# Kernel optimization log

Measured on AMD Instinct MI355X. Metric: run time of the kernel, lower is better.

The kernel has to match this reference:

```python
import jax, jax.numpy as jnp
from jax import lax
import numpy as np

N = 10000      # num_nodes
T = 24         # hist_len
IN_DIM = 16
HID = 128
HEADS = 4
E = 160000     # num_edges
PRED = 24
NEG_SLOPE = 0.2  # GATv2 LeakyReLU default


def _lstm_layer(xs, wih, whh, bih, bhh):
    # xs: [T, N, D]; PyTorch gate order i, f, g, o
    Hh = whh.shape[1]
    h0 = jnp.zeros((xs.shape[1], Hh), xs.dtype)
    def step(carry, xt):
        h, c = carry
        g = xt @ wih.T + bih + h @ whh.T + bhh
        i, f, gg, o = jnp.split(g, 4, axis=-1)
        c = jax.nn.sigmoid(f) * c + jax.nn.sigmoid(i) * jnp.tanh(gg)
        h = jax.nn.sigmoid(o) * jnp.tanh(c)
        return (h, c), h
    (_, _), out = lax.scan(step, (h0, h0), xs)
    return out  # [T, N, Hh]


def _gatv2(z, src, dst, wl, bl, wr, br, att, bias):
    # PyG GATv2Conv: share_weights=False, concat=True, add_self_loops=False
    n = z.shape[0]
    xl = (z @ wl.T + bl).reshape(n, HEADS, HID)   # source/message transform
    xr = (z @ wr.T + br).reshape(n, HEADS, HID)   # target transform
    e = jax.nn.leaky_relu(xl[src] + xr[dst], NEG_SLOPE)   # [E, H, C]
    score = jnp.einsum('ehc,hc->eh', e, att)              # [E, H]
    smax = jax.ops.segment_max(score, dst, num_segments=n)
    p = jnp.exp(score - smax[dst])
    denom = jax.ops.segment_sum(p, dst, num_segments=n)
    alpha = p / (denom[dst] + 1e-16)                      # segment softmax over in-edges
    out = jax.ops.segment_sum(xl[src] * alpha[:, :, None], dst, num_segments=n)
    return out.reshape(n, HEADS * HID) + bias


def setup_inputs() -> dict:
    key = jax.random.key(0)
    ks = iter(jax.random.split(key, 64))
    def W(shape):
        return jax.random.normal(next(ks), shape, jnp.float32) / np.sqrt(shape[-1])
    inp = {}
    inp['x'] = jax.random.normal(next(ks), (N, T, IN_DIM), jnp.float32)
    inp['edge_index'] = jax.random.randint(next(ks), (2, E), 0, N, jnp.int32)
    inp['mlp_in_w0'] = W((HID, IN_DIM)); inp['mlp_in_b0'] = jnp.zeros((HID,), jnp.float32)
    inp['mlp_in_w1'] = W((HID, HID));    inp['mlp_in_b1'] = jnp.zeros((HID,), jnp.float32)
    for l in range(2):  # nn.LSTM(num_layers = lstm_num_layers*2 = 2)
        inp[f'lstm_wih{l}'] = W((4 * HID, HID))
        inp[f'lstm_whh{l}'] = W((4 * HID, HID))
        inp[f'lstm_bih{l}'] = jnp.zeros((4 * HID,), jnp.float32)
        inp[f'lstm_bhh{l}'] = jnp.zeros((4 * HID,), jnp.float32)
    for l in range(2):  # nGAT_layer = 2
        inp[f'gat{l}_wl'] = W((HEADS * HID, HID))
        inp[f'gat{l}_bl'] = jnp.zeros((HEADS * HID,), jnp.float32)
        inp[f'gat{l}_wr'] = W((HEADS * HID, HID))
        inp[f'gat{l}_br'] = jnp.zeros((HEADS * HID,), jnp.float32)
        inp[f'gat{l}_att'] = W((HEADS, HID))
        inp[f'gat{l}_bias'] = jnp.zeros((HEADS * HID,), jnp.float32)
        inp[f'gat{l}_pw'] = W((HID, HEADS * HID))
        inp[f'gat{l}_pb'] = jnp.zeros((HID,), jnp.float32)
    inp['mlp_out_w0'] = W((HID, HID));  inp['mlp_out_b0'] = jnp.zeros((HID,), jnp.float32)
    inp['mlp_out_w1'] = W((PRED, HID)); inp['mlp_out_b1'] = jnp.zeros((PRED,), jnp.float32)
    return inp


def _forward(x, edge_index, mlp_in_w0, mlp_in_b0, mlp_in_w1, mlp_in_b1,
             lstm_wih0, lstm_whh0, lstm_bih0, lstm_bhh0,
             lstm_wih1, lstm_whh1, lstm_bih1, lstm_bhh1,
             gat0_wl, gat0_bl, gat0_wr, gat0_br, gat0_att, gat0_bias, gat0_pw, gat0_pb,
             gat1_wl, gat1_bl, gat1_wr, gat1_br, gat1_att, gat1_bias, gat1_pw, gat1_pb,
             mlp_out_w0, mlp_out_b0, mlp_out_w1, mlp_out_b1):
    src, dst = edge_index[0], edge_index[1]
    h = jnp.transpose(x, (1, 0, 2))                       # [T, N, in_dim]
    # MLP_layers_in: Linear(in,hid), Linear(hid,hid), ReLU
    h = h @ mlp_in_w0.T + mlp_in_b0
    h = jax.nn.relu(h @ mlp_in_w1.T + mlp_in_b1)
    # 2-layer unidirectional LSTM
    h = _lstm_layer(h, lstm_wih0, lstm_whh0, lstm_bih0, lstm_bhh0)
    h = _lstm_layer(h, lstm_wih1, lstm_whh1, lstm_bih1, lstm_bhh1)
    z = h[-1]                                             # [N, HID] last timestep
    # GAT block x2: GATv2Conv -> Linear(heads*hid, hid) -> ReLU
    z = _gatv2(z, src, dst, gat0_wl, gat0_bl, gat0_wr, gat0_br, gat0_att, gat0_bias)
    z = jax.nn.relu(z @ gat0_pw.T + gat0_pb)
    z = _gatv2(z, src, dst, gat1_wl, gat1_bl, gat1_wr, gat1_br, gat1_att, gat1_bias)
    z = jax.nn.relu(z @ gat1_pw.T + gat1_pb)
    # MLP_layers_out: Linear(hid,hid), ReLU, Linear(hid, pred_len)
    z = jax.nn.relu(z @ mlp_out_w0.T + mlp_out_b0)
    return z @ mlp_out_w1.T + mlp_out_b1                  # [N, PRED]


def reference(x, edge_index, mlp_in_w0, mlp_in_b0, mlp_in_w1, mlp_in_b1,
              lstm_wih0, lstm_whh0, lstm_bih0, lstm_bhh0,
              lstm_wih1, lstm_whh1, lstm_bih1, lstm_bhh1,
              gat0_wl, gat0_bl, gat0_wr, gat0_br, gat0_att, gat0_bias, gat0_pw, gat0_pb,
              gat1_wl, gat1_bl, gat1_wr, gat1_br, gat1_att, gat1_bias, gat1_pw, gat1_pb,
              mlp_out_w0, mlp_out_b0, mlp_out_w1, mlp_out_b1):
    return _forward(x, edge_index, mlp_in_w0, mlp_in_b0, mlp_in_w1, mlp_in_b1,
                    lstm_wih0, lstm_whh0, lstm_bih0, lstm_bhh0,
                    lstm_wih1, lstm_whh1, lstm_bih1, lstm_bhh1,
                    gat0_wl, gat0_bl, gat0_wr, gat0_br, gat0_att, gat0_bias, gat0_pw, gat0_pb,
                    gat1_wl, gat1_bl, gat1_wr, gat1_br, gat1_att, gat1_bias, gat1_pw, gat1_pb,
                    mlp_out_w0, mlp_out_b0, mlp_out_w1, mlp_out_b1)
```

## Files before the change

kernel.cpp:

```cpp
#include <hip/hip_runtime.h>
#include <hip/hip_bf16.h>

#define NNODES 10000
#define TLEN 24
#define INDIM 16
#define HID 128
#define GDIM 512

typedef __hip_bfloat16 bf16;
typedef short v8s __attribute__((ext_vector_type(8)));
typedef float v4f __attribute__((ext_vector_type(4)));

__device__ inline float u2f(unsigned u){ return __uint_as_float(u); }

__device__ inline void unpack8(uint4 v, float* f){
  f[0]=u2f(v.x<<16); f[1]=u2f(v.x&0xFFFF0000u);
  f[2]=u2f(v.y<<16); f[3]=u2f(v.y&0xFFFF0000u);
  f[4]=u2f(v.z<<16); f[5]=u2f(v.z&0xFFFF0000u);
  f[6]=u2f(v.w<<16); f[7]=u2f(v.w&0xFFFF0000u);
}

__device__ inline float fsig(float x){
  return __builtin_amdgcn_rcpf(1.f + __expf(-x));
}
__device__ inline float ftanh(float x){
  float e = __expf(2.f*x);
  return 1.f - 2.f*__builtin_amdgcn_rcpf(e + 1.f);
}

__global__ __launch_bounds__(256) void conv_w_k(
    const float* s0, const float* s1, const float* s2, const float* s3,
    const float* s4, const float* s5, const float* s6, const float* s7,
    const float* s8, const float* s9, const float* s10,
    bf16* __restrict__ dst, int* __restrict__ deg)
{
  int idx = blockIdx.x*256 + threadIdx.x;
  if (idx < NNODES) deg[idx] = 0;
  if (idx >= 671744) return;
  int c = idx >> 16;
  float v;
  if (c < 10){
    const float* srcs[10] = {s0,s1,s2,s3,s4,s5,s6,s7,s8,s9};
    v = srcs[c][idx & 0xFFFF];
  } else {
    v = s10[idx - 655360];
  }
  dst[idx] = __float2bfloat16(v);
}

__global__ __launch_bounds__(256) void prep_w_k(
    const float* __restrict__ miw0, const float* __restrict__ mib0,
    const float* __restrict__ miw1, const float* __restrict__ mib1,
    const float* __restrict__ bih0, const float* __restrict__ bhh0,
    const float* __restrict__ bih1, const float* __restrict__ bhh1,
    const float* __restrict__ bl0, const float* __restrict__ br0,
    const float* __restrict__ bl1, const float* __restrict__ br1,
    float* __restrict__ Wp, float* __restrict__ bp,
    float* __restrict__ bsum, float* __restrict__ gblr)
{
  int t = threadIdx.x;
  int b = blockIdx.x;
  if (b < 8){
    int idx = b*256 + t;
    int j = idx >> 4, d = idx & 15;
    float s = 0.f;
    for (int k=0;k<HID;k++) s += miw1[j*HID+k] * miw0[k*INDIM+d];
    Wp[idx] = s;
    return;
  }
  if (t < HID){
    float s = mib1[t];
    for (int k=0;k<HID;k++) s += miw1[t*HID+k] * mib0[k];
    bp[t] = s;
  }
  for (int i = t; i < GDIM; i += 256){
    bsum[i]        = bih0[i] + bhh0[i];
    bsum[GDIM + i] = bih1[i] + bhh1[i];
  }
  for (int i = t; i < GDIM; i += 256){
    gblr[i]          = bl0[i];
    gblr[GDIM + i]   = br0[i];
    gblr[1024 + i]   = bl1[i];
    gblr[1536 + i]   = br1[i];
  }
}

__global__ __launch_bounds__(256) void mlp_in_k(
    const float* __restrict__ x, const float* __restrict__ Wp,
    const float* __restrict__ bp, bf16* __restrict__ X0)
{
  __shared__ __align__(16) float xs[64*16];
  const int tid = threadIdx.x;
  const int m0 = blockIdx.x*64;
  {
    int row = tid >> 2, q = tid & 3;
    int m = m0 + row;
    int t = m / NNODES, n = m - t*NNODES;
    float4 v = *(const float4*)(x + ((size_t)n*TLEN + t)*INDIM + q*4);
    *(float4*)(xs + row*16 + q*4) = v;
  }
  const int j = tid & 127;
  const int half = tid >> 7;
  const float* wr = Wp + j*INDIM;
  float4 w0 = *(const float4*)(wr);
  float4 w1 = *(const float4*)(wr + 4);
  float4 w2 = *(const float4*)(wr + 8);
  float4 w3 = *(const float4*)(wr + 12);
  float bj = bp[j];
  __syncthreads();
  #pragma unroll 4
  for (int mi=0; mi<32; mi++){
    int row = mi*2 + half;
    const float* xr = xs + row*16;
    float4 a0 = *(const float4*)(xr);
    float4 a1 = *(const float4*)(xr + 4);
    float4 a2 = *(const float4*)(xr + 8);
    float4 a3 = *(const float4*)(xr + 12);
    float s = bj
      + a0.x*w0.x + a0.y*w0.y + a0.z*w0.z + a0.w*w0.w
      + a1.x*w1.x + a1.y*w1.y + a1.z*w1.z + a1.w*w1.w
      + a2.x*w2.x + a2.y*w2.y + a2.z*w2.z + a2.w*w2.w
      + a3.x*w3.x + a3.y*w3.y + a3.z*w3.z + a3.w*w3.w;
    s = s > 0.f ? s : 0.f;
    X0[(size_t)(m0+row)*HID + j] = __float2bfloat16(s);
  }
}

template<int WRITE_ALL>
__global__ __launch_bounds__(512) void lstm48(
    const bf16* __restrict__ Xin, const bf16* __restrict__ Wih,
    const bf16* __restrict__ Whh, const float* __restrict__ bias,
    bf16* __restrict__ out)
{
  __shared__ __align__(16) bf16 hs[2][48*136];
  __shared__ __align__(16) bf16 xs[2][48*136];
  const int tid = threadIdx.x;
  const int lane = tid & 63, w = tid >> 6;
  const int r16 = lane & 15, quad = lane >> 4;
  const int m0 = blockIdx.x*48;

  v8s wbi[4][4], wbh[4][4];
  #pragma unroll
  for (int g=0; g<4; g++)
    #pragma unroll
    for (int kc=0; kc<4; kc++){
      size_t o = (size_t)(g*HID + w*16 + r16)*HID + kc*32 + quad*8;
      wbi[g][kc] = *(const v8s*)(Wih + o);
      wbh[g][kc] = *(const v8s*)(Whh + o);
    }
  float bg[4];
  #pragma unroll
  for (int g=0; g<4; g++) bg[g] = bias[g*HID + w*16 + r16];

  const int row0 = tid >> 4;
  const int c8   = (tid & 15) * 8;
  const int row1 = 32 + (tid >> 4);
  const int gr0 = m0 + row0;
  const int gr1 = m0 + row1;
  const int gr0c = gr0 < NNODES ? gr0 : NNODES-1;
  const int gr1c = gr1 < NNODES ? gr1 : NNODES-1;
  const bf16* ldp0 = Xin + (size_t)gr0c*HID + c8;
  const bf16* ldp1 = Xin + (size_t)gr1c*HID + c8;
  bf16* stp0 = (bf16*)Xin + (size_t)gr0*HID + c8;
  bf16* stp1 = (bf16*)Xin + (size_t)gr1*HID + c8;
  const size_t TS = (size_t)NNODES*HID;

  for (int i = tid; i < 816; i += 512)
    *(uint4*)((char*)hs[0] + i*16) = make_uint4(0,0,0,0);

  {
    uint4 a = *(const uint4*)ldp0;
    *(uint4*)(&xs[0][row0*136 + c8]) = a;
    if (tid < 256){
      uint4 b = *(const uint4*)ldp1;
      *(uint4*)(&xs[0][row1*136 + c8]) = b;
    }
  }
  __syncthreads();

  float c[3][4];
  #pragma unroll
  for (int tl=0; tl<3; tl++)
    #pragma unroll
    for (int r=0; r<4; r++) c[tl][r] = 0.f;

  const int fb = r16*136 + quad*8;

  #pragma unroll 1
  for (int t=0; t<TLEN; t++){
    const int cur = t & 1, nxt = cur ^ 1;
    const bf16* xrd = xs[cur];
    const bf16* hrd = hs[cur];
    bf16* hwr = hs[nxt];

    const int tn = (t+1 < TLEN) ? t+1 : TLEN-1;
    uint4 xa = *(const uint4*)(ldp0 + (size_t)tn*TS);
    uint4 xb;
    if (tid < 256) xb = *(const uint4*)(ldp1 + (size_t)tn*TS);

    #pragma unroll
    for (int tl=0; tl<3; tl++){
      v4f acc[4];
      #pragma unroll
      for (int g=0; g<4; g++) acc[g] = (v4f)0.f;

      #pragma unroll
      for (int kc=0; kc<4; kc++){
        v8s av = *(const v8s*)(xrd + tl*2176 + fb + kc*32);
        #pragma unroll
        for (int g=0; g<4; g++)
          acc[g] = __builtin_amdgcn_mfma_f32_16x16x32_bf16(av, wbi[g][kc], acc[g], 0, 0, 0);
      }
      #pragma unroll
      for (int kc=0; kc<4; kc++){
        v8s hv = *(const v8s*)(hrd + tl*2176 + fb + kc*32);
        #pragma unroll
        for (int g=0; g<4; g++)
          acc[g] = __builtin_amdgcn_mfma_f32_16x16x32_bf16(hv, wbh[g][kc], acc[g], 0, 0, 0);
      }

      #pragma unroll
      for (int r=0; r<4; r++){
        float iv = acc[0][r] + bg[0];
        float fv = acc[1][r] + bg[1];
        float gv = acc[2][r] + bg[2];
        float ov = acc[3][r] + bg[3];
        float ig = fsig(iv), fg = fsig(fv);
        float gg = ftanh(gv), og = fsig(ov);
        float cn = fg*c[tl][r] + ig*gg;
        c[tl][r] = cn;
        hwr[(tl*16 + quad*4 + r)*136 + w*16 + r16] = __float2bfloat16(og*ftanh(cn));
      }
    }

    *(uint4*)(&xs[nxt][row0*136 + c8]) = xa;
    if (tid < 256) *(uint4*)(&xs[nxt][row1*136 + c8]) = xb;

    __syncthreads();

    if (WRITE_ALL){
      uint4 h0 = *(const uint4*)(&hwr[row0*136 + c8]);
      if (gr0 < NNODES) *(uint4*)(stp0 + (size_t)t*TS) = h0;
      if (tid < 256){
        uint4 h1v = *(const uint4*)(&hwr[row1*136 + c8]);
        if (gr1 < NNODES) *(uint4*)(stp1 + (size_t)t*TS) = h1v;
      }
    }
  }

  if (!WRITE_ALL){
    const bf16* hf = hs[TLEN & 1];
    uint4 h0 = *(const uint4*)(&hf[row0*136 + c8]);
    if (gr0 < NNODES) *(uint4*)(out + (size_t)gr0*HID + c8) = h0;
    if (tid < 256){
      uint4 h1v = *(const uint4*)(&hf[row1*136 + c8]);
      if (gr1 < NNODES) *(uint4*)(out + (size_t)gr1*HID + c8) = h1v;
    }
  }
}

template<int ACT>
__global__ __launch_bounds__(256) void gemm_bt(
    const bf16* __restrict__ A, const bf16* __restrict__ B,
    const float* __restrict__ bias, bf16* __restrict__ C,
    int M, int N, int K)
{
  __shared__ __align__(16) bf16 As[128*40];
  __shared__ __align__(16) bf16 Bs[128*40];
  const int tid = threadIdx.x;
  const int m0 = blockIdx.x*128, n0 = blockIdx.y*128;
  const int lane = tid & 63, wave = tid >> 6;
  const int r16 = lane & 15, quad = lane >> 4;

  v4f acc[2][8];
  #pragma unroll
  for (int a=0;a<2;a++)
    #pragma unroll
    for (int b=0;b<8;b++) acc[a][b] = (v4f)0.f;

  for (int k0=0; k0<K; k0+=32){
    #pragma unroll
    for (int i=0;i<2;i++){
      int li = tid + i*256;
      int row = li >> 2, q4 = li & 3;
      uint4 va = make_uint4(0,0,0,0);
      int gm = m0 + row;
      if (gm < M) va = *(const uint4*)(A + (size_t)gm*K + k0 + q4*8);
      *(uint4*)(As + row*40 + q4*8) = va;
      uint4 vb = make_uint4(0,0,0,0);
      int gn = n0 + row;
      if (gn < N) vb = *(const uint4*)(B + (size_t)gn*K + k0 + q4*8);
      *(uint4*)(Bs + row*40 + q4*8) = vb;
    }
    __syncthreads();
    v8s av[2], bv[8];
    #pragma unroll
    for (int mi=0;mi<2;mi++)
      av[mi] = *(const v8s*)(As + (wave*32 + mi*16 + r16)*40 + quad*8);
    #pragma unroll
    for (int ni=0;ni<8;ni++)
      bv[ni] = *(const v8s*)(Bs + (ni*16 + r16)*40 + quad*8);
    #pragma unroll
    for (int mi=0;mi<2;mi++)
      #pragma unroll
      for (int ni=0;ni<8;ni++)
        acc[mi][ni] = __builtin_amdgcn_mfma_f32_16x16x32_bf16(av[mi], bv[ni], acc[mi][ni], 0, 0, 0);
    __syncthreads();
  }

  #pragma unroll
  for (int mi=0;mi<2;mi++){
    #pragma unroll
    for (int r=0;r<4;r++){
      int row = m0 + wave*32 + mi*16 + quad*4 + r;
      if (row >= M) continue;
      #pragma unroll
      for (int ni=0;ni<8;ni++){
        int col = n0 + ni*16 + r16;
        float v = acc[mi][ni][r] + bias[col];
        if (ACT == 1) v = v > 0.f ? v : 0.f;
        C[(size_t)row*N + col] = __float2bfloat16(v);
      }
    }
  }
}

template<int ACT>
__global__ __launch_bounds__(256) void gemm_bt64(
    const bf16* __restrict__ A, const bf16* __restrict__ B,
    const float* __restrict__ bias, bf16* __restrict__ C,
    int M, int K)
{
  __shared__ __align__(16) bf16 As[64*40];
  __shared__ __align__(16) bf16 Bs[128*40];
  const int tid = threadIdx.x;
  const int m0 = blockIdx.x*64;
  const int lane = tid & 63, wave = tid >> 6;
  const int r16 = lane & 15, quad = lane >> 4;

  v4f acc[8];
  #pragma unroll
  for (int b=0;b<8;b++) acc[b] = (v4f)0.f;

  for (int k0=0; k0<K; k0+=32){
    {
      int row = tid >> 2, q4 = tid & 3;
      uint4 va = make_uint4(0,0,0,0);
      int gm = m0 + row;
      if (gm < M) va = *(const uint4*)(A + (size_t)gm*K + k0 + q4*8);
      *(uint4*)(As + row*40 + q4*8) = va;
    }
    #pragma unroll
    for (int i=0;i<2;i++){
      int li = tid + i*256;
      int row = li >> 2, q4 = li & 3;
      uint4 vb = *(const uint4*)(B + (size_t)row*K + k0 + q4*8);
      *(uint4*)(Bs + row*40 + q4*8) = vb;
    }
    __syncthreads();
    v8s av, bv[8];
    av = *(const v8s*)(As + (wave*16 + r16)*40 + quad*8);
    #pragma unroll
    for (int ni=0;ni<8;ni++)
      bv[ni] = *(const v8s*)(Bs + (ni*16 + r16)*40 + quad*8);
    #pragma unroll
    for (int ni=0;ni<8;ni++)
      acc[ni] = __builtin_amdgcn_mfma_f32_16x16x32_bf16(av, bv[ni], acc[ni], 0, 0, 0);
    __syncthreads();
  }

  #pragma unroll
  for (int r=0;r<4;r++){
    int row = m0 + wave*16 + quad*4 + r;
    if (row >= M) continue;
    #pragma unroll
    for (int ni=0;ni<8;ni++){
      int col = ni*16 + r16;
      float v = acc[ni][r] + bias[col];
      if (ACT == 1) v = v > 0.f ? v : 0.f;
      C[(size_t)row*HID + col] = __float2bfloat16(v);
    }
  }
}

__global__ __launch_bounds__(256) void mlp_out_fused_k(
    const bf16* __restrict__ A, const bf16* __restrict__ B,
    const float* __restrict__ bias, const float* __restrict__ w1,
    const float* __restrict__ b1, float* __restrict__ out, int M)
{
  __shared__ __align__(16) bf16 As[64*40];
  __shared__ __align__(16) bf16 Bs[128*40];
  __shared__ __align__(16) bf16 o0s[64*136];
  const int tid = threadIdx.x;
  const int m0 = blockIdx.x*64;
  const int lane = tid & 63, wave = tid >> 6;
  const int r16 = lane & 15, quad = lane >> 4;

  v4f acc[8];
  #pragma unroll
  for (int b=0;b<8;b++) acc[b] = (v4f)0.f;

  for (int k0=0; k0<HID; k0+=32){
    {
      int row = tid >> 2, q4 = tid & 3;
      uint4 va = make_uint4(0,0,0,0);
      int gm = m0 + row;
      if (gm < M) va = *(const uint4*)(A + (size_t)gm*HID + k0 + q4*8);
      *(uint4*)(As + row*40 + q4*8) = va;
    }
    #pragma unroll
    for (int i=0;i<2;i++){
      int li = tid + i*256;
      int row = li >> 2, q4 = li & 3;
      uint4 vb = *(const uint4*)(B + (size_t)row*HID + k0 + q4*8);
      *(uint4*)(Bs + row*40 + q4*8) = vb;
    }
    __syncthreads();
    v8s av, bv[8];
    av = *(const v8s*)(As + (wave*16 + r16)*40 + quad*8);
    #pragma unroll
    for (int ni=0;ni<8;ni++)
      bv[ni] = *(const v8s*)(Bs + (ni*16 + r16)*40 + quad*8);
    #pragma unroll
    for (int ni=0;ni<8;ni++)
      acc[ni] = __builtin_amdgcn_mfma_f32_16x16x32_bf16(av, bv[ni], acc[ni], 0, 0, 0);
    __syncthreads();
  }

  #pragma unroll
  for (int r=0;r<4;r++){
    int row = wave*16 + quad*4 + r;
    #pragma unroll
    for (int ni=0;ni<8;ni++){
      int col = ni*16 + r16;
      float v = acc[ni][r] + bias[col];
      v = v > 0.f ? v : 0.f;
      o0s[row*136 + col] = __float2bfloat16(v);
    }
  }
  __syncthreads();

  for (int idx = tid; idx < 64*24; idx += 256){
    int row = idx / 24, j = idx - row*24;
    if (m0 + row >= M) continue;
    const bf16* ar = o0s + row*136;
    const float* wr = w1 + j*HID;
    float s = b1[j];
    for (int k=0;k<HID;k+=8){
      float fa[8];
      unpack8(*(const uint4*)(ar+k), fa);
      float4 w0 = *(const float4*)(wr + k);
      float4 w1v = *(const float4*)(wr + k + 4);
      s += fa[0]*w0.x + fa[1]*w0.y + fa[2]*w0.z + fa[3]*w0.w
         + fa[4]*w1v.x + fa[5]*w1v.y + fa[6]*w1v.z + fa[7]*w1v.w;
    }
    out[(size_t)(m0+row)*24 + j] = s;
  }
}

__global__ void deg_count_k(const int* __restrict__ dst, int* __restrict__ deg, int E){
  int e = blockIdx.x*256 + threadIdx.x;
  if (e < E){
    unsigned d = (unsigned)dst[e];
    if (d < (unsigned)NNODES) atomicAdd(&deg[d], 1);
  }
}

__global__ void scan_k(const int* __restrict__ deg, int* __restrict__ offs,
                       int* __restrict__ cursor, int n)
{
  __shared__ int part[256];
  __shared__ int base[256];
  int t = threadIdx.x;
  int lo = t*40, hi = lo+40;
  if (lo > n) lo = n;
  if (hi > n) hi = n;
  int s = 0;
  for (int i=lo;i<hi;i++) s += deg[i];
  part[t] = s;
  __syncthreads();
  if (t == 0){
    int run=0;
    for (int i=0;i<256;i++){ base[i]=run; run+=part[i]; }
    offs[n] = run;
  }
  __syncthreads();
  int run = base[t];
  for (int i=lo;i<hi;i++){ offs[i]=run; cursor[i]=run; run += deg[i]; }
}

__global__ void fill_k(const int* __restrict__ src, const int* __restrict__ dst,
                       int* __restrict__ cursor, int* __restrict__ srcs, int E){
  int e = blockIdx.x*256 + threadIdx.x;
  if (e < E){
    unsigned d = (unsigned)dst[e];
    if (d < (unsigned)NNODES){
      int p = atomicAdd(&cursor[d], 1);
      unsigned s = (unsigned)src[e];
      srcs[p] = (s < (unsigned)NNODES) ? (int)s : 0;
    }
  }
}

__global__ __launch_bounds__(256) void gat_onl(
    const int* __restrict__ offs, const int* __restrict__ srcs,
    const bf16* __restrict__ xc, const float* __restrict__ att,
    const float* __restrict__ gbias, bf16* __restrict__ agg)
{
  int d = blockIdx.x*4 + (threadIdx.x >> 6);
  if (d >= NNODES) return;
  int lane = threadIdx.x & 63;
  float fr[8];
  unpack8(*(const uint4*)(xc + (size_t)d*1024 + 512 + lane*8), fr);
  float4 a0 = *(const float4*)(att + lane*8);
  float4 a1 = *(const float4*)(att + lane*8 + 4);
  float fa[8] = {a0.x,a0.y,a0.z,a0.w,a1.x,a1.y,a1.z,a1.w};
  int i0 = offs[d], i1 = offs[d+1];

  float m = -3.4e38f, den = 0.f;
  float acc[8] = {0,0,0,0,0,0,0,0};

  if (i0 < i1){
    uint4 r0 = *(const uint4*)(xc + (size_t)srcs[i0]*1024 + lane*8);
    uint4 r1 = r0;
    if (i0+1 < i1) r1 = *(const uint4*)(xc + (size_t)srcs[i0+1]*1024 + lane*8);
    for (int i=i0; i<i1; i++){
      uint4 r2 = r1;
      if (i+2 < i1) r2 = *(const uint4*)(xc + (size_t)srcs[i+2]*1024 + lane*8);
      float fl[8];
      unpack8(r0, fl);
      float p = 0.f;
      #pragma unroll
      for (int q=0;q<8;q++){
        float v = fl[q] + fr[q];
        v = v > 0.f ? v : 0.2f*v;
        p += v*fa[q];
      }
      p += __shfl_xor(p, 1); p += __shfl_xor(p, 2);
      p += __shfl_xor(p, 4); p += __shfl_xor(p, 8);
      float mn = fmaxf(m, p);
      float corr = __expf(m - mn);
      float w = __expf(p - mn);
      den = den*corr + w;
      #pragma unroll
      for (int q=0;q<8;q++) acc[q] = acc[q]*corr + w*fl[q];
      m = mn;
      r0 = r1; r1 = r2;
    }
  }
  float r = 1.f/(den + 1e-16f);
  float4 b0 = *(const float4*)(gbias + lane*8);
  float4 b1 = *(const float4*)(gbias + lane*8 + 4);
  float fb[8] = {b0.x,b0.y,b0.z,b0.w,b1.x,b1.y,b1.z,b1.w};
  #pragma unroll
  for (int q=0;q<8;q++)
    agg[(size_t)d*GDIM + lane*8 + q] = __float2bfloat16(acc[q]*r + fb[q]);
}


extern "C" void kernel_launch(void* const* d_in, const int* in_sizes, int n_in,
                              void* d_out, int out_size, void* d_ws, size_t ws_size,
                              hipStream_t stream)
{
  const float* x   = (const float*)d_in[0];
  const int*   ei  = (const int*)d_in[1];
  const int E = in_sizes[1] / 2;
  const int* srcp = ei;
  const int* dstp = ei + E;

  const float* miw0 = (const float*)d_in[2];
  const float* mib0 = (const float*)d_in[3];
  const float* miw1 = (const float*)d_in[4];
  const float* mib1 = (const float*)d_in[5];
  const float* wih0 = (const float*)d_in[6];
  const float* whh0 = (const float*)d_in[7];
  const float* bih0 = (const float*)d_in[8];
  const float* bhh0 = (const float*)d_in[9];
  const float* wih1 = (const float*)d_in[10];
  const float* whh1 = (const float*)d_in[11];
  const float* bih1 = (const float*)d_in[12];
  const float* bhh1 = (const float*)d_in[13];
  const float* g_wl[2]   = {(const float*)d_in[14], (const float*)d_in[22]};
  const float* g_bl[2]   = {(const float*)d_in[15], (const float*)d_in[23]};
  const float* g_wr[2]   = {(const float*)d_in[16], (const float*)d_in[24]};
  const float* g_br[2]   = {(const float*)d_in[17], (const float*)d_in[25]};
  const float* g_att[2]  = {(const float*)d_in[18], (const float*)d_in[26]};
  const float* g_bias[2] = {(const float*)d_in[19], (const float*)d_in[27]};
  const float* g_pw[2]   = {(const float*)d_in[20], (const float*)d_in[28]};
  const float* g_pb[2]   = {(const float*)d_in[21], (const float*)d_in[29]};
  const float* mow0 = (const float*)d_in[30];
  const float* mob0 = (const float*)d_in[31];
  const float* mow1 = (const float*)d_in[32];
  const float* mob1 = (const float*)d_in[33];
  (void)n_in; (void)out_size; (void)ws_size;

  char* base = (char*)d_ws;
  size_t off = 0;
  auto carve = [&](size_t n)->char*{
    char* p = base + off;
    off = (off + n + 255) & ~(size_t)255;
    return p;
  };
  char*  X0r = carve((size_t)TLEN*NNODES*HID*2);
  bf16*  zf  = (bf16*)carve((size_t)NNODES*HID*2);
  float* Wp  = (float*)carve(HID*INDIM*4);
  float* bp  = (float*)carve(HID*4);
  float* bsum= (float*)carve(2*GDIM*4);
  float* gblr= (float*)carve(2*1024*4);
  bf16*  wbf = (bf16*)carve((size_t)671744*2);
  int*   offsb = (int*)carve((size_t)(NNODES+1)*4);
  int*   curs  = (int*)carve((size_t)NNODES*4);
  int*   srcs  = (int*)carve((size_t)E*4);
  int*   deg   = (int*)carve((size_t)NNODES*4);
  bf16*  agg   = (bf16*)carve((size_t)NNODES*GDIM*2);

  const bf16* wih0b = wbf + 0;
  const bf16* whh0b = wbf + 65536;
  const bf16* wih1b = wbf + 131072;
  const bf16* whh1b = wbf + 196608;
  const bf16* wlr0b = wbf + 262144;
  const bf16* pw0b  = wbf + 393216;
  const bf16* wlr1b = wbf + 458752;
  const bf16* pw1b  = wbf + 589824;
  const bf16* mow0b = wbf + 655360;
  const bf16* wlrb[2] = {wlr0b, wlr1b};
  const bf16* pwb[2]  = {pw0b, pw1b};

  bf16* X0 = (bf16*)X0r;
  bf16* xc = (bf16*)X0r;
  bf16* z2 = (bf16*)(X0r + 20480000);
  bf16* z3 = (bf16*)(X0r + 23040000);

  conv_w_k<<<2624, 256, 0, stream>>>(wih0, whh0, wih1, whh1,
                                     g_wl[0], g_wr[0], g_pw[0],
                                     g_wl[1], g_wr[1], g_pw[1], mow0, wbf, deg);
  prep_w_k<<<9, 256, 0, stream>>>(miw0, mib0, miw1, mib1,
                                  bih0, bhh0, bih1, bhh1,
                                  g_bl[0], g_br[0], g_bl[1], g_br[1],
                                  Wp, bp, bsum, gblr);

  mlp_in_k<<<(TLEN*NNODES)/64, 256, 0, stream>>>(x, Wp, bp, X0);

  deg_count_k<<<(E+255)/256, 256, 0, stream>>>(dstp, deg, E);
  scan_k<<<1, 256, 0, stream>>>(deg, offsb, curs, NNODES);
  fill_k<<<(E+255)/256, 256, 0, stream>>>(srcp, dstp, curs, srcs, E);

  const int NBL48 = (NNODES + 47) / 48;
  lstm48<1><<<NBL48, 512, 0, stream>>>(X0, wih0b, whh0b, bsum, nullptr);
  lstm48<0><<<NBL48, 512, 0, stream>>>(X0, wih1b, whh1b, bsum + GDIM, zf);

  const bf16* zin = zf;
  bf16* zouts[2] = {z2, z3};
  const int NB64 = (NNODES + 63) / 64;
  for (int l=0; l<2; l++){
    gemm_bt<0><<<dim3(79,8), 256, 0, stream>>>(zin, wlrb[l], gblr + l*1024, xc, NNODES, 1024, HID);
    gat_onl<<<(NNODES+3)/4, 256, 0, stream>>>(offsb, srcs, xc, g_att[l], g_bias[l], agg);
    gemm_bt64<1><<<NB64, 256, 0, stream>>>(agg, pwb[l], g_pb[l], zouts[l], NNODES, GDIM);
    zin = zouts[l];
  }

  mlp_out_fused_k<<<NB64, 256, 0, stream>>>(z3, mow0b, mob0, mow1, mob1,
                                            (float*)d_out, NNODES);
}
```

Measured before the change: 526.4 us.

## Fuse graph CSR build into prep/mlp_in, rewrite LSTM activations, widen GEMM N tile

Degree counting moves into extra blocks of prep_w_k and the CSR fill into mlp_in_k, which removes two kernel launches. The LSTM cell math is rewritten so the input gate and tanh(g) share one reciprocal, as do the output gate and tanh(c), cutting rcp instructions on the sequential critical path. The projection GEMM tile grows from 128x128 to 128x256 with twice the accumulators per thread. The wider tile halves the grid and raises register pressure, and the fused atomics add work to mlp_in.

```diff
diff --git a/kernel.cpp b/kernel.cpp
--- a/kernel.cpp
+++ b/kernel.cpp
@@ -12,20 +12,13 @@
 typedef float v4f __attribute__((ext_vector_type(4)));
 
 __device__ inline float u2f(unsigned u){ return __uint_as_float(u); }
+__device__ inline float frcp(float x){ return __builtin_amdgcn_rcpf(x); }
 
 __device__ inline void unpack8(uint4 v, float* f){
   f[0]=u2f(v.x<<16); f[1]=u2f(v.x&0xFFFF0000u);
   f[2]=u2f(v.y<<16); f[3]=u2f(v.y&0xFFFF0000u);
   f[4]=u2f(v.z<<16); f[5]=u2f(v.z&0xFFFF0000u);
   f[6]=u2f(v.w<<16); f[7]=u2f(v.w&0xFFFF0000u);
-}
-
-__device__ inline float fsig(float x){
-  return __builtin_amdgcn_rcpf(1.f + __expf(-x));
-}
-__device__ inline float ftanh(float x){
-  float e = __expf(2.f*x);
-  return 1.f - 2.f*__builtin_amdgcn_rcpf(e + 1.f);
 }
 
 __global__ __launch_bounds__(256) void conv_w_k(
@@ -56,10 +49,19 @@
     const float* __restrict__ bl0, const float* __restrict__ br0,
     const float* __restrict__ bl1, const float* __restrict__ br1,
     float* __restrict__ Wp, float* __restrict__ bp,
-    float* __restrict__ bsum, float* __restrict__ gblr)
+    float* __restrict__ bsum, float* __restrict__ gblr,
+    const int* __restrict__ dst, int* __restrict__ deg, int E)
 {
   int t = threadIdx.x;
   int b = blockIdx.x;
+  if (b >= 9){
+    int e = (b-9)*256 + t;
+    if (e < E){
+      unsigned d = (unsigned)dst[e];
+      if (d < (unsigned)NNODES) atomicAdd(&deg[d], 1);
+    }
+    return;
+  }
   if (b < 8){
     int idx = b*256 + t;
     int j = idx >> 4, d = idx & 15;
@@ -85,9 +87,34 @@
   }
 }
 
+__global__ void scan_k(const int* __restrict__ deg, int* __restrict__ offs,
+                       int* __restrict__ cursor, int n)
+{
+  __shared__ int part[256];
+  __shared__ int base[256];
+  int t = threadIdx.x;
+  int lo = t*40, hi = lo+40;
+  if (lo > n) lo = n;
+  if (hi > n) hi = n;
+  int s = 0;
+  for (int i=lo;i<hi;i++) s += deg[i];
+  part[t] = s;
+  __syncthreads();
+  if (t == 0){
+    int run=0;
+    for (int i=0;i<256;i++){ base[i]=run; run+=part[i]; }
+    offs[n] = run;
+  }
+  __syncthreads();
+  int run = base[t];
+  for (int i=lo;i<hi;i++){ offs[i]=run; cursor[i]=run; run += deg[i]; }
+}
+
 __global__ __launch_bounds__(256) void mlp_in_k(
     const float* __restrict__ x, const float* __restrict__ Wp,
-    const float* __restrict__ bp, bf16* __restrict__ X0)
+    const float* __restrict__ bp, bf16* __restrict__ X0,
+    const int* __restrict__ srcp, const int* __restrict__ dstp,
+    int* __restrict__ curs, int* __restrict__ srcs, int E)
 {
   __shared__ __align__(16) float xs[64*16];
   const int tid = threadIdx.x;
@@ -98,6 +125,17 @@
     int t = m / NNODES, n = m - t*NNODES;
     float4 v = *(const float4*)(x + ((size_t)n*TLEN + t)*INDIM + q*4);
     *(float4*)(xs + row*16 + q*4) = v;
+  }
+  {
+    int gid = blockIdx.x*256 + tid;
+    if (gid < E){
+      unsigned d = (unsigned)dstp[gid];
+      if (d < (unsigned)NNODES){
+        int p = atomicAdd(&curs[d], 1);
+        unsigned s = (unsigned)srcp[gid];
+        srcs[p] = (s < (unsigned)NNODES) ? (int)s : 0;
+      }
+    }
   }
   const int j = tid & 127;
   const int half = tid >> 7;
@@ -225,11 +263,16 @@
         float fv = acc[1][r] + bg[1];
         float gv = acc[2][r] + bg[2];
         float ov = acc[3][r] + bg[3];
-        float ig = fsig(iv), fg = fsig(fv);
-        float gg = ftanh(gv), og = fsig(ov);
-        float cn = fg*c[tl][r] + ig*gg;
+        float sf = frcp(1.f + __expf(-fv));
+        float ei = __expf(-iv);
+        float tg = __expf(-2.f*fabsf(gv));
+        float itg = copysignf((1.f - tg)*frcp((1.f + ei)*(1.f + tg)), gv);
+        float cn = sf*c[tl][r] + itg;
         c[tl][r] = cn;
-        hwr[(tl*16 + quad*4 + r)*136 + w*16 + r16] = __float2bfloat16(og*ftanh(cn));
+        float eo = __expf(-ov);
+        float tc = __expf(-2.f*fabsf(cn));
+        float hh = copysignf((1.f - tc)*frcp((1.f + eo)*(1.f + tc)), cn);
+        hwr[(tl*16 + quad*4 + r)*136 + w*16 + r16] = __float2bfloat16(hh);
       }
     }
 
@@ -266,17 +309,17 @@
     int M, int N, int K)
 {
   __shared__ __align__(16) bf16 As[128*40];
-  __shared__ __align__(16) bf16 Bs[128*40];
+  __shared__ __align__(16) bf16 Bs[256*40];
   const int tid = threadIdx.x;
-  const int m0 = blockIdx.x*128, n0 = blockIdx.y*128;
+  const int m0 = blockIdx.x*128, n0 = blockIdx.y*256;
   const int lane = tid & 63, wave = tid >> 6;
   const int r16 = lane & 15, quad = lane >> 4;
 
-  v4f acc[2][8];
+  v4f acc[2][16];
   #pragma unroll
   for (int a=0;a<2;a++)
     #pragma unroll
-    for (int b=0;b<8;b++) acc[a][b] = (v4f)0.f;
+    for (int b=0;b<16;b++) acc[a][b] = (v4f)0.f;
 
   for (int k0=0; k0<K; k0+=32){
     #pragma unroll
@@ -287,24 +330,33 @@
       int gm = m0 + row;
       if (gm < M) va = *(const uint4*)(A + (size_t)gm*K + k0 + q4*8);
       *(uint4*)(As + row*40 + q4*8) = va;
+    }
+    #pragma unroll
+    for (int i=0;i<4;i++){
+      int li = tid + i*256;
+      int row = li >> 2, q4 = li & 3;
       uint4 vb = make_uint4(0,0,0,0);
       int gn = n0 + row;
       if (gn < N) vb = *(const uint4*)(B + (size_t)gn*K + k0 + q4*8);
       *(uint4*)(Bs + row*40 + q4*8) = vb;
     }
     __syncthreads();
-    v8s av[2], bv[8];
+    v8s av[2];
     #pragma unroll
     for (int mi=0;mi<2;mi++)
       av[mi] = *(const v8s*)(As + (wave*32 + mi*16 + r16)*40 + quad*8);
     #pragma unroll
-    for (int ni=0;ni<8;ni++)
-      bv[ni] = *(const v8s*)(Bs + (ni*16 + r16)*40 + quad*8);
-    #pragma unroll
-    for (int mi=0;mi<2;mi++)
+    for (int h=0;h<2;h++){
+      v8s bv[8];
       #pragma unroll
       for (int ni=0;ni<8;ni++)
-        acc[mi][ni] = __builtin_amdgcn_mfma_f32_16x16x32_bf16(av[mi], bv[ni], acc[mi][ni], 0, 0, 0);
+        bv[ni] = *(const v8s*)(Bs + ((h*8+ni)*16 + r16)*40 + quad*8);
+      #pragma unroll
+      for (int mi=0;mi<2;mi++)
+        #pragma unroll
+        for (int ni=0;ni<8;ni++)
+          acc[mi][h*8+ni] = __builtin_amdgcn_mfma_f32_16x16x32_bf16(av[mi], bv[ni], acc[mi][h*8+ni], 0, 0, 0);
+    }
     __syncthreads();
   }
 
@@ -315,7 +367,7 @@
       int row = m0 + wave*32 + mi*16 + quad*4 + r;
       if (row >= M) continue;
       #pragma unroll
-      for (int ni=0;ni<8;ni++){
+      for (int ni=0;ni<16;ni++){
         int col = n0 + ni*16 + r16;
         float v = acc[mi][ni][r] + bias[col];
         if (ACT == 1) v = v > 0.f ? v : 0.f;
@@ -455,50 +507,6 @@
          + fa[4]*w1v.x + fa[5]*w1v.y + fa[6]*w1v.z + fa[7]*w1v.w;
     }
     out[(size_t)(m0+row)*24 + j] = s;
-  }
-}
-
-__global__ void deg_count_k(const int* __restrict__ dst, int* __restrict__ deg, int E){
-  int e = blockIdx.x*256 + threadIdx.x;
-  if (e < E){
-    unsigned d = (unsigned)dst[e];
-    if (d < (unsigned)NNODES) atomicAdd(&deg[d], 1);
-  }
-}
-
-__global__ void scan_k(const int* __restrict__ deg, int* __restrict__ offs,
-                       int* __restrict__ cursor, int n)
-{
-  __shared__ int part[256];
-  __shared__ int base[256];
-  int t = threadIdx.x;
-  int lo = t*40, hi = lo+40;
-  if (lo > n) lo = n;
-  if (hi > n) hi = n;
-  int s = 0;
-  for (int i=lo;i<hi;i++) s += deg[i];
-  part[t] = s;
-  __syncthreads();
-  if (t == 0){
-    int run=0;
-    for (int i=0;i<256;i++){ base[i]=run; run+=part[i]; }
-    offs[n] = run;
-  }
-  __syncthreads();
-  int run = base[t];
-  for (int i=lo;i<hi;i++){ offs[i]=run; cursor[i]=run; run += deg[i]; }
-}
-
-__global__ void fill_k(const int* __restrict__ src, const int* __restrict__ dst,
-                       int* __restrict__ cursor, int* __restrict__ srcs, int E){
-  int e = blockIdx.x*256 + threadIdx.x;
-  if (e < E){
-    unsigned d = (unsigned)dst[e];
-    if (d < (unsigned)NNODES){
-      int p = atomicAdd(&cursor[d], 1);
-      unsigned s = (unsigned)src[e];
-      srcs[p] = (s < (unsigned)NNODES) ? (int)s : 0;
-    }
   }
 }
 
@@ -634,16 +642,14 @@
   conv_w_k<<<2624, 256, 0, stream>>>(wih0, whh0, wih1, whh1,
                                      g_wl[0], g_wr[0], g_pw[0],
                                      g_wl[1], g_wr[1], g_pw[1], mow0, wbf, deg);
-  prep_w_k<<<9, 256, 0, stream>>>(miw0, mib0, miw1, mib1,
+  prep_w_k<<<9 + (E+255)/256, 256, 0, stream>>>(miw0, mib0, miw1, mib1,
                                   bih0, bhh0, bih1, bhh1,
                                   g_bl[0], g_br[0], g_bl[1], g_br[1],
-                                  Wp, bp, bsum, gblr);
-
-  mlp_in_k<<<(TLEN*NNODES)/64, 256, 0, stream>>>(x, Wp, bp, X0);
-
-  deg_count_k<<<(E+255)/256, 256, 0, stream>>>(dstp, deg, E);
+                                  Wp, bp, bsum, gblr, dstp, deg, E);
   scan_k<<<1, 256, 0, stream>>>(deg, offsb, curs, NNODES);
-  fill_k<<<(E+255)/256, 256, 0, stream>>>(srcp, dstp, curs, srcs, E);
+
+  mlp_in_k<<<(TLEN*NNODES)/64, 256, 0, stream>>>(x, Wp, bp, X0,
+                                                 srcp, dstp, curs, srcs, E);
 
   const int NBL48 = (NNODES + 47) / 48;
   lstm48<1><<<NBL48, 512, 0, stream>>>(X0, wih0b, whh0b, bsum, nullptr);
@@ -653,7 +659,7 @@
   bf16* zouts[2] = {z2, z3};
   const int NB64 = (NNODES + 63) / 64;
   for (int l=0; l<2; l++){
-    gemm_bt<0><<<dim3(79,8), 256, 0, stream>>>(zin, wlrb[l], gblr + l*1024, xc, NNODES, 1024, HID);
+    gemm_bt<0><<<dim3(79,4), 256, 0, stream>>>(zin, wlrb[l], gblr + l*1024, xc, NNODES, 1024, HID);
     gat_onl<<<(NNODES+3)/4, 256, 0, stream>>>(offsb, srcs, xc, g_att[l], g_bias[l], agg);
     gemm_bt64<1><<<NB64, 256, 0, stream>>>(agg, pwb[l], g_pb[l], zouts[l], NNODES, GDIM);
     zin = zouts[l];
```

After: 545.4 us. 1.04x slower.
